# Kernel optimization log

Measured on AMD Instinct MI355X. Metric: run time of the kernel, lower is better.

## Reference

```python
import jax, jax.numpy as jnp
import numpy as np

HASH_SIZE = 256      # hash_table_size
OFFSET_SIZE = 64     # offset_table_size
FEAT = 8             # feature_channels
N_QUERIES = 4_000_000
DOMAIN = 1024


def setup_inputs() -> dict:
    key = jax.random.key(0)
    k1, k2, k3 = jax.random.split(key, 3)
    coords = jax.random.randint(k1, (N_QUERIES, 3), 0, DOMAIN, dtype=jnp.int32)
    hash_table = jax.random.normal(k2, (HASH_SIZE, HASH_SIZE, HASH_SIZE, FEAT), dtype=jnp.float32)
    # uint8 offsets in [0, 256); stored as int32 for jax indexing arithmetic
    offset_table = jax.random.randint(k3, (OFFSET_SIZE, OFFSET_SIZE, OFFSET_SIZE, 3), 0, 256, dtype=jnp.int32)
    m0 = jnp.ones((3,), dtype=jnp.float32)
    m1 = jnp.ones((3,), dtype=jnp.float32)
    return {"coords": coords, "hash_table": hash_table, "offset_table": offset_table,
            "m0": m0, "m1": m1}


def reference(coords, hash_table, offset_table, m0, m1):
    # Stage 1: offset-table lookup. torch: (x * m1).long() % offset_table_size
    oidx = (coords.astype(jnp.float32) * m1).astype(jnp.int32) % OFFSET_SIZE  # [N,3]
    offsets = offset_table[oidx[:, 0], oidx[:, 1], oidx[:, 2]]                # [N,3]
    # Stage 2: perfect-hash index. torch: ((x*m0).long() + offset) % hash_table_size
    h0 = (coords.astype(jnp.float32) * m0).astype(jnp.int32)
    hidx = (h0 + offsets) % HASH_SIZE                                          # [N,3]
    # Feature gather from the hash table
    features = hash_table[hidx[:, 0], hidx[:, 1], hidx[:, 2]]                  # [N,FEAT]
    return features
```

## Files before the change

### kernel.cpp

```cpp
#include <hip/hip_runtime.h>

#define HASH_SIZE 256
#define OFFSET_SIZE 64
#define FEAT 8

__global__ void __launch_bounds__(256)
psh_kernel(const int* __restrict__ coords,
           const float* __restrict__ hash_table,
           const int* __restrict__ offset_table,
           const float* __restrict__ m0,
           const float* __restrict__ m1,
           float* __restrict__ out,
           int n) {
    int i = blockIdx.x * blockDim.x + threadIdx.x;
    if (i >= n) return;

    float m0x = m0[0], m0y = m0[1], m0z = m0[2];
    float m1x = m1[0], m1y = m1[1], m1z = m1[2];

    int cx = coords[3 * i + 0];
    int cy = coords[3 * i + 1];
    int cz = coords[3 * i + 2];

    int ox = ((int)((float)cx * m1x)) & (OFFSET_SIZE - 1);
    int oy = ((int)((float)cy * m1y)) & (OFFSET_SIZE - 1);
    int oz = ((int)((float)cz * m1z)) & (OFFSET_SIZE - 1);

    size_t ooff = ((size_t)((ox * OFFSET_SIZE + oy) * OFFSET_SIZE + oz)) * 3;
    int dx = offset_table[ooff + 0];
    int dy = offset_table[ooff + 1];
    int dz = offset_table[ooff + 2];

    int hx = (((int)((float)cx * m0x)) + dx) & (HASH_SIZE - 1);
    int hy = (((int)((float)cy * m0y)) + dy) & (HASH_SIZE - 1);
    int hz = (((int)((float)cz * m0z)) + dz) & (HASH_SIZE - 1);

    size_t hoff = (((size_t)hx * HASH_SIZE + hy) * HASH_SIZE + hz) * FEAT;
    const float4* hp = (const float4*)(hash_table + hoff);
    float4 f0 = hp[0];
    float4 f1 = hp[1];

    float4* op = (float4*)(out + (size_t)i * FEAT);
    op[0] = f0;
    op[1] = f1;
}

extern "C" void kernel_launch(void* const* d_in, const int* in_sizes, int n_in,
                              void* d_out, int out_size, void* d_ws, size_t ws_size,
                              hipStream_t stream) {
    const int*   coords       = (const int*)d_in[0];
    const float* hash_table   = (const float*)d_in[1];
    const int*   offset_table = (const int*)d_in[2];
    const float* m0           = (const float*)d_in[3];
    const float* m1           = (const float*)d_in[4];
    float*       out          = (float*)d_out;

    int n = in_sizes[0] / 3;
    int block = 256;
    int grid = (n + block - 1) / block;
    psh_kernel<<<grid, block, 0, stream>>>(coords, hash_table, offset_table,
                                           m0, m1, out, n);
}
```

Before: 743.4 us.

## Pack offset table into 32-bit words and process four queries per thread

A pre-pass kernel packs the int32 offset table (three values per entry) into one 32-bit word per entry in the workspace, shrinking the offset table from about 3 MB to 1 MB and replacing three scattered loads with one. The main kernel now handles four queries per thread, loading coords as three 16-byte nontemporal vector loads and writing outputs with nontemporal stores, so more gathers are in flight per thread. The packed path runs only if the workspace is large enough, and it adds an extra kernel launch on every call.

New measurement: 936.6 us. 26.0% more time.

```diff
diff --git a/kernel.cpp b/kernel.cpp
--- a/kernel.cpp
+++ b/kernel.cpp
@@ -3,46 +3,123 @@
 #define HASH_SIZE 256
 #define OFFSET_SIZE 64
 #define FEAT 8
+#define OT_ENTRIES (OFFSET_SIZE * OFFSET_SIZE * OFFSET_SIZE)
+
+typedef int   iv4 __attribute__((ext_vector_type(4)));
+typedef float fv4 __attribute__((ext_vector_type(4)));
 
 __global__ void __launch_bounds__(256)
-psh_kernel(const int* __restrict__ coords,
-           const float* __restrict__ hash_table,
-           const int* __restrict__ offset_table,
-           const float* __restrict__ m0,
-           const float* __restrict__ m1,
-           float* __restrict__ out,
-           int n) {
+pack_offsets_kernel(const int* __restrict__ offset_table,
+                    unsigned int* __restrict__ packed) {
     int i = blockIdx.x * blockDim.x + threadIdx.x;
-    if (i >= n) return;
+    if (i >= OT_ENTRIES) return;
+    unsigned dx = (unsigned)offset_table[3 * i + 0] & 255u;
+    unsigned dy = (unsigned)offset_table[3 * i + 1] & 255u;
+    unsigned dz = (unsigned)offset_table[3 * i + 2] & 255u;
+    packed[i] = dx | (dy << 8) | (dz << 16);
+}
+
+template <bool PACKED>
+__global__ void __launch_bounds__(256)
+psh_kernel4(const int* __restrict__ coords,
+            const float* __restrict__ hash_table,
+            const int* __restrict__ offset_table,
+            const unsigned int* __restrict__ offset_packed,
+            const float* __restrict__ m0,
+            const float* __restrict__ m1,
+            float* __restrict__ out,
+            int n) {
+    int t = blockIdx.x * blockDim.x + threadIdx.x;
+    int base = t * 4;
+    if (base >= n) return;
 
     float m0x = m0[0], m0y = m0[1], m0z = m0[2];
     float m1x = m1[0], m1y = m1[1], m1z = m1[2];
 
-    int cx = coords[3 * i + 0];
-    int cy = coords[3 * i + 1];
-    int cz = coords[3 * i + 2];
+    if (base + 4 <= n) {
+        const iv4* c4 = (const iv4*)(coords + (size_t)base * 3);
+        iv4 va = __builtin_nontemporal_load(c4 + 0);
+        iv4 vb = __builtin_nontemporal_load(c4 + 1);
+        iv4 vc = __builtin_nontemporal_load(c4 + 2);
+        int cx[4] = {va.x, va.w, vb.z, vc.y};
+        int cy[4] = {va.y, vb.x, vb.w, vc.z};
+        int cz[4] = {va.z, vb.y, vc.x, vc.w};
 
-    int ox = ((int)((float)cx * m1x)) & (OFFSET_SIZE - 1);
-    int oy = ((int)((float)cy * m1y)) & (OFFSET_SIZE - 1);
-    int oz = ((int)((float)cz * m1z)) & (OFFSET_SIZE - 1);
+        int dx[4], dy[4], dz[4];
+        if (PACKED) {
+            unsigned pk[4];
+#pragma unroll
+            for (int q = 0; q < 4; ++q) {
+                int ox = ((int)((float)cx[q] * m1x)) & (OFFSET_SIZE - 1);
+                int oy = ((int)((float)cy[q] * m1y)) & (OFFSET_SIZE - 1);
+                int oz = ((int)((float)cz[q] * m1z)) & (OFFSET_SIZE - 1);
+                pk[q] = offset_packed[(ox * OFFSET_SIZE + oy) * OFFSET_SIZE + oz];
+            }
+#pragma unroll
+            for (int q = 0; q < 4; ++q) {
+                dx[q] = (int)(pk[q] & 255u);
+                dy[q] = (int)((pk[q] >> 8) & 255u);
+                dz[q] = (int)((pk[q] >> 16) & 255u);
+            }
+        } else {
+#pragma unroll
+            for (int q = 0; q < 4; ++q) {
+                int ox = ((int)((float)cx[q] * m1x)) & (OFFSET_SIZE - 1);
+                int oy = ((int)((float)cy[q] * m1y)) & (OFFSET_SIZE - 1);
+                int oz = ((int)((float)cz[q] * m1z)) & (OFFSET_SIZE - 1);
+                size_t ooff = ((size_t)((ox * OFFSET_SIZE + oy) * OFFSET_SIZE + oz)) * 3;
+                dx[q] = offset_table[ooff + 0];
+                dy[q] = offset_table[ooff + 1];
+                dz[q] = offset_table[ooff + 2];
+            }
+        }
 
-    size_t ooff = ((size_t)((ox * OFFSET_SIZE + oy) * OFFSET_SIZE + oz)) * 3;
-    int dx = offset_table[ooff + 0];
-    int dy = offset_table[ooff + 1];
-    int dz = offset_table[ooff + 2];
+        fv4 f[8];
+#pragma unroll
+        for (int q = 0; q < 4; ++q) {
+            int hx = (((int)((float)cx[q] * m0x)) + dx[q]) & (HASH_SIZE - 1);
+            int hy = (((int)((float)cy[q] * m0y)) + dy[q]) & (HASH_SIZE - 1);
+            int hz = (((int)((float)cz[q] * m0z)) + dz[q]) & (HASH_SIZE - 1);
+            const fv4* hp = (const fv4*)(hash_table +
+                (((size_t)hx * HASH_SIZE + hy) * HASH_SIZE + hz) * FEAT);
+            f[2 * q + 0] = hp[0];
+            f[2 * q + 1] = hp[1];
+        }
 
-    int hx = (((int)((float)cx * m0x)) + dx) & (HASH_SIZE - 1);
-    int hy = (((int)((float)cy * m0y)) + dy) & (HASH_SIZE - 1);
-    int hz = (((int)((float)cz * m0z)) + dz) & (HASH_SIZE - 1);
-
-    size_t hoff = (((size_t)hx * HASH_SIZE + hy) * HASH_SIZE + hz) * FEAT;
-    const float4* hp = (const float4*)(hash_table + hoff);
-    float4 f0 = hp[0];
-    float4 f1 = hp[1];
-
-    float4* op = (float4*)(out + (size_t)i * FEAT);
-    op[0] = f0;
-    op[1] = f1;
+        fv4* o4 = (fv4*)(out + (size_t)base * FEAT);
+#pragma unroll
+        for (int j = 0; j < 8; ++j)
+            __builtin_nontemporal_store(f[j], o4 + j);
+    } else {
+        for (int i = base; i < n; ++i) {
+            int cx = coords[3 * i + 0];
+            int cy = coords[3 * i + 1];
+            int cz = coords[3 * i + 2];
+            int ox = ((int)((float)cx * m1x)) & (OFFSET_SIZE - 1);
+            int oy = ((int)((float)cy * m1y)) & (OFFSET_SIZE - 1);
+            int oz = ((int)((float)cz * m1z)) & (OFFSET_SIZE - 1);
+            int dx, dy, dz;
+            if (PACKED) {
+                unsigned pk = offset_packed[(ox * OFFSET_SIZE + oy) * OFFSET_SIZE + oz];
+                dx = (int)(pk & 255u);
+                dy = (int)((pk >> 8) & 255u);
+                dz = (int)((pk >> 16) & 255u);
+            } else {
+                size_t ooff = ((size_t)((ox * OFFSET_SIZE + oy) * OFFSET_SIZE + oz)) * 3;
+                dx = offset_table[ooff + 0];
+                dy = offset_table[ooff + 1];
+                dz = offset_table[ooff + 2];
+            }
+            int hx = (((int)((float)cx * m0x)) + dx) & (HASH_SIZE - 1);
+            int hy = (((int)((float)cy * m0y)) + dy) & (HASH_SIZE - 1);
+            int hz = (((int)((float)cz * m0z)) + dz) & (HASH_SIZE - 1);
+            const fv4* hp = (const fv4*)(hash_table +
+                (((size_t)hx * HASH_SIZE + hy) * HASH_SIZE + hz) * FEAT);
+            fv4* o4 = (fv4*)(out + (size_t)i * FEAT);
+            o4[0] = hp[0];
+            o4[1] = hp[1];
+        }
+    }
 }
 
 extern "C" void kernel_launch(void* const* d_in, const int* in_sizes, int n_in,
@@ -56,8 +133,25 @@
     float*       out          = (float*)d_out;
 
     int n = in_sizes[0] / 3;
+
+    size_t need = (size_t)OT_ENTRIES * sizeof(unsigned int);
+    bool packed = (d_ws != nullptr) && (ws_size >= need);
+
+    if (packed) {
+        pack_offsets_kernel<<<(OT_ENTRIES + 255) / 256, 256, 0, stream>>>(
+            offset_table, (unsigned int*)d_ws);
+    }
+
+    int nthreads = (n + 3) / 4;
     int block = 256;
-    int grid = (n + block - 1) / block;
-    psh_kernel<<<grid, block, 0, stream>>>(coords, hash_table, offset_table,
-                                           m0, m1, out, n);
+    int grid = (nthreads + block - 1) / block;
+    if (packed) {
+        psh_kernel4<true><<<grid, block, 0, stream>>>(
+            coords, hash_table, offset_table, (const unsigned int*)d_ws,
+            m0, m1, out, n);
+    } else {
+        psh_kernel4<false><<<grid, block, 0, stream>>>(
+            coords, hash_table, offset_table, nullptr,
+            m0, m1, out, n);
+    }
 }
```
